# Kernel tuning notes

Measured on AMD Instinct MI355X. Metric: run time of the kernel, lower is better.

The kernel has to match this reference:

```python
import jax, jax.numpy as jnp
import numpy as np
import math

N, S, D, C, CLASSES = 512, 256, 512, 1024, 1000


def setup_inputs() -> dict:
    key = jax.random.key(0)
    ks = jax.random.split(key, 9)
    q = jax.random.normal(ks[0], (N, D), dtype=jnp.float32)
    K = jax.random.normal(ks[1], (N, S, D), dtype=jnp.float32)
    V = jax.random.normal(ks[2], (N, S, D), dtype=jnp.float32)
    codebook = jax.random.normal(ks[3], (C, D), dtype=jnp.float32) / math.sqrt(D)
    Wq = jax.random.normal(ks[4], (D, D), dtype=jnp.float32) / math.sqrt(D)
    Wc = jax.random.normal(ks[5], (CLASSES, D), dtype=jnp.float32) / math.sqrt(D)
    bc = jnp.zeros((CLASSES,), dtype=jnp.float32)
    Wr = jax.random.normal(ks[6], (D, D), dtype=jnp.float32) / math.sqrt(D)
    br = jnp.zeros((D,), dtype=jnp.float32)
    return {"q": q, "K": K, "V": V, "codebook": codebook,
            "Wq": Wq, "Wc": Wc, "bc": bc, "Wr": Wr, "br": br}


def reference(q, K, V, codebook, Wq, Wc, bc, Wr, br):
    d = q.shape[-1]
    scale = math.sqrt(d)
    # query projection (Linear, no bias): q @ Wq^T
    q_proj = jnp.einsum('nd,ed->ne', q, Wq)
    # query-to-codebook soft assignment [n, c]
    code_weights = jax.nn.softmax(jnp.einsum('nd,cd->nc', q_proj, codebook) / scale, axis=-1)
    # slot-to-codebook soft assignment [n, s, c]
    slot_code_weights = jax.nn.softmax(jnp.einsum('nsd,cd->nsc', K, codebook) / scale, axis=-1)
    # fused: einsum('nc,ncd->nd', code_weights, einsum('nsc,nsd->ncd', ...))
    # == contract c first to get per-slot weights [n, s], then mix V.
    effective_weights = jnp.einsum('nc,nsc->ns', code_weights, slot_code_weights)
    summary = jnp.einsum('ns,nsd->nd', effective_weights, V)
    logits = jnp.einsum('nd,kd->nk', summary, Wc) + bc
    recon = jnp.einsum('nd,ed->ne', summary, Wr) + br
    return (logits, recon, effective_weights)
```

## Files before the change

### kernel.cpp

```cpp
#include <hip/hip_runtime.h>
#include <hip/hip_bf16.h>
#include <stdint.h>


typedef float  f32x4 __attribute__((ext_vector_type(4)));
typedef float  f32x2 __attribute__((ext_vector_type(2)));
typedef short  s16x8 __attribute__((ext_vector_type(8)));

__device__ __forceinline__ unsigned short f2bf(float x){
  unsigned u = __float_as_uint(x);
  u += 0x7fffu + ((u >> 16) & 1u);
  return (unsigned short)(u >> 16);
}
__device__ __forceinline__ float hsum4(f32x4 v){ return v[0]+v[1]+v[2]+v[3]; }

static constexpr float INV_SCALE = 0.04419417382415922f;

__global__ __launch_bounds__(256) void k_prep(const float* __restrict__ cb,
                                              unsigned short* __restrict__ cbB,
                                              const float* __restrict__ q,
                                              const float* __restrict__ Wq,
                                              float* __restrict__ cw){
  __shared__ __align__(16) float qrow[2][512];
  __shared__ __align__(16) float qproj[2][512];
  __shared__ float ev[2][1024];
  __shared__ float red[256];
  __shared__ float tot[2];
  const int t = threadIdx.x;

  if (blockIdx.x < 256){
    const int g = blockIdx.x*256 + t;
    const int ks8 = g & 3;
    const int cr  = (g >> 2) & 31;
    const int kk  = (g >> 7) & 15;
    const int p   = g >> 11;
    const int c = p*32 + cr;
    const int k = kk*32 + ks8*8;
    const float* src = cb + (size_t)c*512 + k;
    const f32x4 v0 = *(const f32x4*)(src);
    const f32x4 v1 = *(const f32x4*)(src + 4);
    s16x8 o;
    o[0]=(short)f2bf(v0[0]*INV_SCALE); o[1]=(short)f2bf(v0[1]*INV_SCALE);
    o[2]=(short)f2bf(v0[2]*INV_SCALE); o[3]=(short)f2bf(v0[3]*INV_SCALE);
    o[4]=(short)f2bf(v1[0]*INV_SCALE); o[5]=(short)f2bf(v1[1]*INV_SCALE);
    o[6]=(short)f2bf(v1[2]*INV_SCALE); o[7]=(short)f2bf(v1[3]*INV_SCALE);
    *(s16x8*)(cbB + (size_t)g*8) = o;
    return;
  }

  const int n0 = (blockIdx.x - 256)*2;
  #pragma unroll
  for (int j = 0; j < 4; ++j){
    const int o = t + 256*j; const int ni = o >> 9, d = o & 511;
    qrow[ni][d] = q[(size_t)(n0+ni)*512 + d];
  }
  __syncthreads();
  {
    const f32x4* q0 = (const f32x4*)qrow[0];
    const f32x4* q1 = (const f32x4*)qrow[1];
    #pragma unroll 1
    for (int j = 0; j < 2; ++j){
      const int e = t + 256*j;
      const f32x4* w4 = (const f32x4*)(Wq + (size_t)e*512);
      f32x4 a0={0,0,0,0},a1={0,0,0,0};
      for (int d = 0; d < 128; ++d){
        const f32x4 wv = w4[d];
        a0 += wv*q0[d]; a1 += wv*q1[d];
      }
      qproj[0][e]=hsum4(a0); qproj[1][e]=hsum4(a1);
    }
  }
  __syncthreads();
  {
    const f32x4* p0 = (const f32x4*)qproj[0];
    const f32x4* p1 = (const f32x4*)qproj[1];
    #pragma unroll 1
    for (int j = 0; j < 4; ++j){
      const int c = t + 256*j;
      const f32x4* c4 = (const f32x4*)(cb + (size_t)c*512);
      f32x4 a0={0,0,0,0},a1={0,0,0,0};
      for (int d = 0; d < 128; ++d){
        const f32x4 wv = c4[d];
        a0 += wv*p0[d]; a1 += wv*p1[d];
      }
      ev[0][c] = __expf(hsum4(a0)*INV_SCALE);
      ev[1][c] = __expf(hsum4(a1)*INV_SCALE);
    }
  }
  __syncthreads();
  for (int ni = 0; ni < 2; ++ni){
    red[t] = ev[ni][t] + ev[ni][t+256] + ev[ni][t+512] + ev[ni][t+768];
    __syncthreads();
    for (int off = 128; off > 0; off >>= 1){
      if (t < off) red[t] += red[t+off];
      __syncthreads();
    }
    if (t == 0) tot[ni] = red[0];
    __syncthreads();
  }
  #pragma unroll
  for (int j = 0; j < 8; ++j){
    const int o = t + 256*j; const int ni = o >> 10, c = o & 1023;
    cw[(size_t)(n0+ni)*1024 + c] = ev[ni][c] / tot[ni];
  }
}

template<bool FUSE_V>
__global__ __launch_bounds__(512, 4) void k_scores(const float* __restrict__ Kt,
                                                   const unsigned short* __restrict__ cbB,
                                                   const float* __restrict__ cw,
                                                   float* __restrict__ ew_out,
                                                   const float* __restrict__ Vp,
                                                   float* __restrict__ partial){
  __shared__ __align__(16) short sA[64*512];
  __shared__ float cwl[1024];
  __shared__ float pe[8][64];
  __shared__ float pw[8][64];
  __shared__ float ewl[64];

  const int t    = threadIdx.x;
  const int lane = t & 63;
  const int w    = t >> 6;
  const int m0   = blockIdx.x * 64;
  const int n    = m0 >> 8;

  {
    const int row = t >> 3;
    const float* src = Kt + (size_t)(m0 + row) * 512;
    #pragma unroll
    for (int j = 0; j < 8; ++j){
      const int slot = (t & 7) + 8*j;
      const f32x4 v0 = *(const f32x4*)(src + slot*8);
      const f32x4 v1 = *(const f32x4*)(src + slot*8 + 4);
      s16x8 o;
      o[0]=(short)f2bf(v0[0]); o[1]=(short)f2bf(v0[1]); o[2]=(short)f2bf(v0[2]); o[3]=(short)f2bf(v0[3]);
      o[4]=(short)f2bf(v1[0]); o[5]=(short)f2bf(v1[1]); o[6]=(short)f2bf(v1[2]); o[7]=(short)f2bf(v1[3]);
      const int sp = slot ^ (row & 7);
      *(s16x8*)&sA[row*512 + sp*8] = o;
    }
  }
  cwl[t]       = cw[(size_t)n*1024 + t];
  cwl[t + 512] = cw[(size_t)n*1024 + t + 512];
  pe[w][lane] = 0.f;
  pw[w][lane] = 0.f;
  __syncthreads();

  const int kg = lane >> 4;
  const int lr = lane & 15;
  const int rot = blockIdx.x & 3;

  #pragma unroll 1
  for (int p = 0; p < 4; ++p){
    const int ci = (p + rot) & 3;
    f32x4 acc[4][2];
    #pragma unroll
    for (int fr = 0; fr < 4; ++fr)
      #pragma unroll
      for (int fc = 0; fc < 2; ++fc) acc[fr][fc] = (f32x4){0.f,0.f,0.f,0.f};

    const unsigned short* pbase = cbB + ((size_t)(ci*8 + w))*16384;
    const int loff = lr*32 + kg*8;

    s16x8 a[2][4], b[4][2];
    #pragma unroll
    for (int s = 0; s < 2; ++s){
      const int kb = (((s + w) & 7)) * 2;
      #pragma unroll
      for (int u = 0; u < 2; ++u)
        #pragma unroll
        for (int fc = 0; fc < 2; ++fc)
          b[2*s + u][fc] = *(const s16x8*)(pbase + (size_t)(kb + u)*1024 + fc*512 + loff);
    }

    #pragma unroll
    for (int jj = 0; jj < 8; ++jj){
      const int kk0 = (((jj + w) & 7)) * 2;
      if (jj < 7) asm volatile("s_waitcnt vmcnt(4)" ::: "memory");
      else        asm volatile("s_waitcnt vmcnt(0)" ::: "memory");
      __builtin_amdgcn_sched_barrier(0);
      #pragma unroll
      for (int u = 0; u < 2; ++u)
        #pragma unroll
        for (int fr = 0; fr < 4; ++fr){
          const int row = fr*16 + lr;
          const int sp  = ((kk0 + u)*4 + kg) ^ (row & 7);
          a[u][fr] = *(const s16x8*)&sA[row*512 + sp*8];
        }
      const int base = (jj & 1) * 2;
      __builtin_amdgcn_s_setprio(1);
      #pragma unroll
      for (int u = 0; u < 2; ++u)
        #pragma unroll
        for (int fr = 0; fr < 4; ++fr)
          #pragma unroll
          for (int fc = 0; fc < 2; ++fc)
            acc[fr][fc] = __builtin_amdgcn_mfma_f32_16x16x32_bf16(a[u][fr], b[base + u][fc], acc[fr][fc], 0, 0, 0);
      __builtin_amdgcn_s_setprio(0);
      __builtin_amdgcn_sched_barrier(0);
      if (jj < 6){
        const int kn = (((jj + 2 + w) & 7)) * 2;
        #pragma unroll
        for (int u = 0; u < 2; ++u)
          #pragma unroll
          for (int fc = 0; fc < 2; ++fc)
            b[base + u][fc] = *(const s16x8*)(pbase + (size_t)(kn + u)*1024 + fc*512 + loff);
      }
    }

    const float cwv0 = cwl[ci*256 + w*32 + 0*16 + lr];
    const float cwv1 = cwl[ci*256 + w*32 + 1*16 + lr];
    #pragma unroll
    for (int fr = 0; fr < 4; ++fr){
      float es[4], ws[4];
      #pragma unroll
      for (int r = 0; r < 4; ++r){
        const float e0 = __expf(acc[fr][0][r]);
        const float e1 = __expf(acc[fr][1][r]);
        es[r] = e0 + e1;
        ws[r] = e0 * cwv0 + e1 * cwv1;
      }
      #pragma unroll
      for (int r = 0; r < 4; ++r){
        float a0 = es[r], b0 = ws[r];
        #pragma unroll
        for (int m = 1; m < 16; m <<= 1){
          a0 += __shfl_xor(a0, m, 64);
          b0 += __shfl_xor(b0, m, 64);
        }
        if (lr == 0){
          const int row = fr*16 + kg*4 + r;
          pe[w][row] += a0;
          pw[w][row] += b0;
        }
      }
    }
  }

  __syncthreads();
  if (t < 64){
    float se = 0.f, sw = 0.f;
    #pragma unroll
    for (int i = 0; i < 8; ++i){ se += pe[i][t]; sw += pw[i][t]; }
    const float e = sw / se;
    ew_out[m0 + t] = e;
    ewl[t] = e;
  }

  if constexpr (FUSE_V){
    __syncthreads();
    float* psum = (float*)sA;
    const int sh = t >> 7;
    const int dq = (t & 127) * 4;
    const float* vb = Vp + (size_t)m0*512 + dq;
    f32x4 av = {0.f,0.f,0.f,0.f};
    #pragma unroll
    for (int i = 0; i < 16; ++i){
      const int s = sh*16 + i;
      av += ewl[s] * *(const f32x4*)(vb + (size_t)s*512);
    }
    *(f32x4*)&psum[sh*512 + dq] = av;
    __syncthreads();
    if (t < 128){
      const int d4 = t*4;
      f32x4 r = *(f32x4*)&psum[d4];
      r += *(f32x4*)&psum[512 + d4];
      r += *(f32x4*)&psum[1024 + d4];
      r += *(f32x4*)&psum[1536 + d4];
      *(f32x4*)&partial[(size_t)blockIdx.x*512 + d4] = r;
    }
  }
}

__global__ __launch_bounds__(256) void k_summary(const float* __restrict__ V,
                                                 const float* __restrict__ ew,
                                                 float* __restrict__ sm){
  __shared__ float e[256];
  __shared__ f32x4 red[3][64];
  const int t = threadIdx.x;
  const int lane = t & 63, w = t >> 6;
  const int n = blockIdx.x >> 1;
  const int d0 = (blockIdx.x & 1) * 256;
  e[t] = ew[(size_t)n*256 + t];
  __syncthreads();
  const float* vb = V + (size_t)n*131072 + d0 + lane*4;
  f32x4 acc = {0.f,0.f,0.f,0.f};
  #pragma unroll 8
  for (int s = w; s < 256; s += 4){
    const f32x4 v = *(const f32x4*)(vb + (size_t)s*512);
    acc += e[s] * v;
  }
  if (w > 0) red[w-1][lane] = acc;
  __syncthreads();
  if (w == 0){
    acc += red[0][lane] + red[1][lane] + red[2][lane];
    *(f32x4*)(sm + (size_t)n*512 + d0 + lane*4) = acc;
  }
}

template<bool FUSED>
__global__ __launch_bounds__(256) void k_readout(const float* __restrict__ src,
                                                 const float* __restrict__ Wc,
                                                 const float* __restrict__ bc,
                                                 const float* __restrict__ Wr,
                                                 const float* __restrict__ br,
                                                 float* __restrict__ logits,
                                                 float* __restrict__ recon){
  __shared__ __align__(16) float sl[8][512];
  const int t = threadIdx.x;
  const int nb  = blockIdx.x >> 2;
  const int wsl = blockIdx.x & 3;
  const int n0 = nb * 8;
  #pragma unroll
  for (int j = 0; j < 16; ++j){
    const int o = t + 256*j; const int ni = o >> 9, d = o & 511;
    if (FUSED){
      const float* pb = src + (size_t)(n0+ni)*2048 + d;
      sl[ni][d] = pb[0] + pb[512] + pb[1024] + pb[1536];
    } else {
      sl[ni][d] = src[(size_t)(n0+ni)*512 + d];
    }
  }
  __syncthreads();
  #pragma unroll 1
  for (int j = 0; j < 2; ++j){
    const int rel = t + 256*j;
    if (rel >= 378) continue;
    const int o = wsl*378 + rel;
    const bool isl = o < 1000;
    const float* wrow = isl ? (Wc + (size_t)o*512) : (Wr + (size_t)(o-1000)*512);
    const float bias  = isl ? bc[o] : br[o-1000];
    const f32x4* w4 = (const f32x4*)wrow;
    f32x4 av[8];
    #pragma unroll
    for (int ni = 0; ni < 8; ++ni) av[ni] = (f32x4){0.f,0.f,0.f,0.f};
    for (int d = 0; d < 128; ++d){
      const f32x4 wv = w4[d];
      #pragma unroll
      for (int ni = 0; ni < 8; ++ni)
        av[ni] += wv * ((const f32x4*)sl[ni])[d];
    }
    #pragma unroll
    for (int ni = 0; ni < 8; ++ni){
      const float r = hsum4(av[ni]) + bias;
      if (isl) logits[(size_t)(n0+ni)*1000 + o] = r;
      else     recon [(size_t)(n0+ni)*512 + (o-1000)] = r;
    }
  }
}

extern "C" void kernel_launch(void* const* d_in, const int* in_sizes, int n_in,
                              void* d_out, int out_size, void* d_ws, size_t ws_size,
                              hipStream_t stream) {
  const float* q  = (const float*)d_in[0];
  const float* K  = (const float*)d_in[1];
  const float* V  = (const float*)d_in[2];
  const float* cb = (const float*)d_in[3];
  const float* Wq = (const float*)d_in[4];
  const float* Wc = (const float*)d_in[5];
  const float* bc = (const float*)d_in[6];
  const float* Wr = (const float*)d_in[7];
  const float* br = (const float*)d_in[8];

  float* out    = (float*)d_out;
  float* logits = out;
  float* recon  = out + 512*1000;
  float* ew     = out + 512*1000 + 512*512;

  char* wsb = (char*)d_ws;
  unsigned short* cbB = (unsigned short*)wsb;
  float* cw   = (float*)(wsb + (1u<<20));
  float* aux  = (float*)(wsb + 3u*(1u<<20));

  const bool fused = ws_size >= (size_t)(7u<<20);

  k_prep<<<dim3(512), dim3(256), 0, stream>>>(cb, cbB, q, Wq, cw);
  if (fused){
    k_scores<true><<<dim3(2048), dim3(512), 0, stream>>>(K, cbB, cw, ew, V, aux);
    k_readout<true><<<dim3(256), dim3(256), 0, stream>>>(aux, Wc, bc, Wr, br, logits, recon);
  } else {
    k_scores<false><<<dim3(2048), dim3(512), 0, stream>>>(K, cbB, cw, ew, V, aux);
    k_summary<<<dim3(1024), dim3(256), 0, stream>>>(V, ew, aux);
    k_readout<false><<<dim3(256), dim3(256), 0, stream>>>(aux, Wc, bc, Wr, br, logits, recon);
  }
}
```

Measured before the change: 423.8 us.

## Batch eight queries per prep block and restructure MFMA k-loop prefetch

The prep kernel now processes eight query rows per block instead of two, so each Wq and codebook row loaded from global memory is reused across eight queries, and the grid shrinks from 512 to 320 blocks. The scores kernel's inner MFMA loop is rewritten to step through 16 single k-slices in order, double-buffering both the LDS A fragments and the global B fragments with a combined vmcnt/lgkmcnt wait. This drops the per-wave rotated k-order. The wider prep block uses more shared memory (about 68 KB) and registers and has fewer blocks for parallelism, and the shallower B prefetch may expose more global latency.

```diff
diff --git a/kernel.cpp b/kernel.cpp
--- a/kernel.cpp
+++ b/kernel.cpp
@@ -21,11 +21,11 @@
                                               const float* __restrict__ q,
                                               const float* __restrict__ Wq,
                                               float* __restrict__ cw){
-  __shared__ __align__(16) float qrow[2][512];
-  __shared__ __align__(16) float qproj[2][512];
-  __shared__ float ev[2][1024];
+  __shared__ __align__(16) float qrow[8][512];
+  __shared__ __align__(16) float qproj[8][512];
+  __shared__ float ev[8][1024];
   __shared__ float red[256];
-  __shared__ float tot[2];
+  __shared__ float tot[8];
   const int t = threadIdx.x;
 
   if (blockIdx.x < 256){
@@ -48,47 +48,53 @@
     return;
   }
 
-  const int n0 = (blockIdx.x - 256)*2;
+  const int n0 = (blockIdx.x - 256)*8;
   #pragma unroll
-  for (int j = 0; j < 4; ++j){
+  for (int j = 0; j < 16; ++j){
     const int o = t + 256*j; const int ni = o >> 9, d = o & 511;
     qrow[ni][d] = q[(size_t)(n0+ni)*512 + d];
   }
   __syncthreads();
   {
-    const f32x4* q0 = (const f32x4*)qrow[0];
-    const f32x4* q1 = (const f32x4*)qrow[1];
     #pragma unroll 1
     for (int j = 0; j < 2; ++j){
       const int e = t + 256*j;
       const f32x4* w4 = (const f32x4*)(Wq + (size_t)e*512);
-      f32x4 a0={0,0,0,0},a1={0,0,0,0};
+      f32x4 av[8];
+      #pragma unroll
+      for (int ni = 0; ni < 8; ++ni) av[ni] = (f32x4){0,0,0,0};
       for (int d = 0; d < 128; ++d){
         const f32x4 wv = w4[d];
-        a0 += wv*q0[d]; a1 += wv*q1[d];
-      }
-      qproj[0][e]=hsum4(a0); qproj[1][e]=hsum4(a1);
+        #pragma unroll
+        for (int ni = 0; ni < 8; ++ni)
+          av[ni] += wv * ((const f32x4*)qrow[ni])[d];
+      }
+      #pragma unroll
+      for (int ni = 0; ni < 8; ++ni) qproj[ni][e] = hsum4(av[ni]);
     }
   }
   __syncthreads();
   {
-    const f32x4* p0 = (const f32x4*)qproj[0];
-    const f32x4* p1 = (const f32x4*)qproj[1];
     #pragma unroll 1
     for (int j = 0; j < 4; ++j){
       const int c = t + 256*j;
       const f32x4* c4 = (const f32x4*)(cb + (size_t)c*512);
-      f32x4 a0={0,0,0,0},a1={0,0,0,0};
+      f32x4 av[8];
+      #pragma unroll
+      for (int ni = 0; ni < 8; ++ni) av[ni] = (f32x4){0,0,0,0};
       for (int d = 0; d < 128; ++d){
         const f32x4 wv = c4[d];
-        a0 += wv*p0[d]; a1 += wv*p1[d];
-      }
-      ev[0][c] = __expf(hsum4(a0)*INV_SCALE);
-      ev[1][c] = __expf(hsum4(a1)*INV_SCALE);
-    }
-  }
-  __syncthreads();
-  for (int ni = 0; ni < 2; ++ni){
+        #pragma unroll
+        for (int ni = 0; ni < 8; ++ni)
+          av[ni] += wv * ((const f32x4*)qproj[ni])[d];
+      }
+      #pragma unroll
+      for (int ni = 0; ni < 8; ++ni)
+        ev[ni][c] = __expf(hsum4(av[ni])*INV_SCALE);
+    }
+  }
+  __syncthreads();
+  for (int ni = 0; ni < 8; ++ni){
     red[t] = ev[ni][t] + ev[ni][t+256] + ev[ni][t+512] + ev[ni][t+768];
     __syncthreads();
     for (int off = 128; off > 0; off >>= 1){
@@ -99,7 +105,7 @@
     __syncthreads();
   }
   #pragma unroll
-  for (int j = 0; j < 8; ++j){
+  for (int j = 0; j < 32; ++j){
     const int o = t + 256*j; const int ni = o >> 10, c = o & 1023;
     cw[(size_t)(n0+ni)*1024 + c] = ev[ni][c] / tot[ni];
   }
@@ -161,50 +167,48 @@
     const unsigned short* pbase = cbB + ((size_t)(ci*8 + w))*16384;
     const int loff = lr*32 + kg*8;
 
-    s16x8 a[2][4], b[4][2];
-    #pragma unroll
-    for (int s = 0; s < 2; ++s){
-      const int kb = (((s + w) & 7)) * 2;
-      #pragma unroll
-      for (int u = 0; u < 2; ++u)
+    s16x8 a[2][4], b[2][2];
+    #pragma unroll
+    for (int fc = 0; fc < 2; ++fc)
+      b[0][fc] = *(const s16x8*)(pbase + 0*1024 + fc*512 + loff);
+    #pragma unroll
+    for (int fc = 0; fc < 2; ++fc)
+      b[1][fc] = *(const s16x8*)(pbase + 1*1024 + fc*512 + loff);
+    #pragma unroll
+    for (int u = 0; u < 2; ++u)
+      #pragma unroll
+      for (int fr = 0; fr < 4; ++fr){
+        const int row = fr*16 + lr;
+        const int sp  = (u*4 + kg) ^ (row & 7);
+        a[u][fr] = *(const s16x8*)&sA[row*512 + sp*8];
+      }
+
+    #pragma unroll
+    for (int kk = 0; kk < 16; ++kk){
+      if (kk < 14)      asm volatile("s_waitcnt vmcnt(2) lgkmcnt(4)" ::: "memory");
+      else if (kk == 14) asm volatile("s_waitcnt vmcnt(2) lgkmcnt(4)" ::: "memory");
+      else              asm volatile("s_waitcnt vmcnt(0) lgkmcnt(0)" ::: "memory");
+      __builtin_amdgcn_sched_barrier(0);
+      __builtin_amdgcn_s_setprio(1);
+      #pragma unroll
+      for (int fr = 0; fr < 4; ++fr)
         #pragma unroll
         for (int fc = 0; fc < 2; ++fc)
-          b[2*s + u][fc] = *(const s16x8*)(pbase + (size_t)(kb + u)*1024 + fc*512 + loff);
-    }
-
-    #pragma unroll
-    for (int jj = 0; jj < 8; ++jj){
-      const int kk0 = (((jj + w) & 7)) * 2;
-      if (jj < 7) asm volatile("s_waitcnt vmcnt(4)" ::: "memory");
-      else        asm volatile("s_waitcnt vmcnt(0)" ::: "memory");
+          acc[fr][fc] = __builtin_amdgcn_mfma_f32_16x16x32_bf16(a[kk & 1][fr], b[kk & 1][fc], acc[fr][fc], 0, 0, 0);
+      __builtin_amdgcn_s_setprio(0);
       __builtin_amdgcn_sched_barrier(0);
-      #pragma unroll
-      for (int u = 0; u < 2; ++u)
+      if (kk < 14){
         #pragma unroll
         for (int fr = 0; fr < 4; ++fr){
           const int row = fr*16 + lr;
-          const int sp  = ((kk0 + u)*4 + kg) ^ (row & 7);
-          a[u][fr] = *(const s16x8*)&sA[row*512 + sp*8];
+          const int sp  = ((kk+2)*4 + kg) ^ (row & 7);
+          a[kk & 1][fr] = *(const s16x8*)&sA[row*512 + sp*8];
         }
-      const int base = (jj & 1) * 2;
-      __builtin_amdgcn_s_setprio(1);
-      #pragma unroll
-      for (int u = 0; u < 2; ++u)
-        #pragma unroll
-        for (int fr = 0; fr < 4; ++fr)
-          #pragma unroll
-          for (int fc = 0; fc < 2; ++fc)
-            acc[fr][fc] = __builtin_amdgcn_mfma_f32_16x16x32_bf16(a[u][fr], b[base + u][fc], acc[fr][fc], 0, 0, 0);
-      __builtin_amdgcn_s_setprio(0);
+        #pragma unroll
+        for (int fc = 0; fc < 2; ++fc)
+          b[kk & 1][fc] = *(const s16x8*)(pbase + (size_t)(kk+2)*1024 + fc*512 + loff);
+      }
       __builtin_amdgcn_sched_barrier(0);
-      if (jj < 6){
-        const int kn = (((jj + 2 + w) & 7)) * 2;
-        #pragma unroll
-        for (int u = 0; u < 2; ++u)
-          #pragma unroll
-          for (int fc = 0; fc < 2; ++fc)
-            b[base + u][fc] = *(const s16x8*)(pbase + (size_t)(kn + u)*1024 + fc*512 + loff);
-      }
     }
 
     const float cwv0 = cwl[ci*256 + w*32 + 0*16 + lr];
@@ -373,7 +377,7 @@
 
   const bool fused = ws_size >= (size_t)(7u<<20);
 
-  k_prep<<<dim3(512), dim3(256), 0, stream>>>(cb, cbB, q, Wq, cw);
+  k_prep<<<dim3(320), dim3(256), 0, stream>>>(cb, cbB, q, Wq, cw);
   if (fused){
     k_scores<true><<<dim3(2048), dim3(512), 0, stream>>>(K, cbB, cw, ew, V, aux);
     k_readout<true><<<dim3(256), dim3(256), 0, stream>>>(aux, Wc, bc, Wr, br, logits, recon);
```

Result: faster. 385.7 us (-9.0%).
